# Kernel optimization log

Hardware: AMD Instinct MI355X
Metric: run time of the kernel (lower is better)

## Reference

```python
import jax, jax.numpy as jnp
import numpy as np

NUM_HEADS = 8
OUT_DIM = 32


def setup_inputs() -> dict:
    key = jax.random.key(0)
    k1, k2, k3, k4 = jax.random.split(key, 4)
    B, N, IN = 2048, 64, 256
    h_i_list = jax.random.normal(k1, (B, N, IN), dtype=jnp.float32)
    h_j_list = jax.random.normal(k2, (B, N, IN), dtype=jnp.float32)
    # Linear weight, applied as x @ W (in_dim, num_heads*out_dim)
    W = jax.random.normal(k3, (IN, NUM_HEADS * OUT_DIM), dtype=jnp.float32) * (1.0 / np.sqrt(IN))
    W_att = jax.random.normal(k4, (1, NUM_HEADS, OUT_DIM), dtype=jnp.float32) * 0.1
    return {"h_i_list": h_i_list, "h_j_list": h_j_list, "W": W, "W_att": W_att}


def reference(h_i_list, h_j_list, W, W_att):
    B, N, _ = h_i_list.shape
    H, D = NUM_HEADS, OUT_DIM
    # [B, N, H, D]
    proj_neigh = (h_j_list @ W).reshape(B, N, H, D)
    proj_self = (h_i_list @ W).reshape(B, N, H, D)
    # attention logits: leakyReLU(sum over feature dim) -> [B, N, H]
    e_ij = jax.nn.leaky_relu(((proj_neigh + proj_self) * W_att[None]).sum(-1), 0.2)
    # softmax over neighbor dim (dim=1)
    alpha = jax.nn.softmax(e_ij, axis=1)  # [B, N, H]
    # weighted neighbor sum -> [B, H, D]
    weight_sum = jnp.einsum("bnh,bnhd->bhd", alpha, proj_neigh)
    # concat=True: [B, 1, H*D]
    h_new = weight_sum.reshape(B, 1, H * D)
    return jax.nn.elu(h_new)
```

## Files before the change

kernel.cpp:

```cpp
#include <hip/hip_runtime.h>

#define NN 64
#define IND 256
#define NH 8
#define OD 32

__device__ __forceinline__ unsigned f2bf(float f) {
  unsigned u = __float_as_uint(f);
  return (u + (((u >> 16) & 1u) + 0x7fffu)) >> 16;
}
__device__ __forceinline__ float bflo(unsigned u) { return __uint_as_float(u << 16); }
__device__ __forceinline__ float bfhi(unsigned u) { return __uint_as_float(u & 0xffff0000u); }

__global__ __launch_bounds__(256) void precompute_v(
    const float* __restrict__ W, const float* __restrict__ Watt, float* __restrict__ V) {
  int tid = blockIdx.x * 256 + threadIdx.x;
  if (tid >= IND * NH) return;
  int h = tid >> 8, k = tid & 255;
  float acc = 0.f;
#pragma unroll
  for (int d = 0; d < OD; ++d) acc += W[k * 256 + h * OD + d] * Watt[h * OD + d];
  V[h * 256 + k] = acc;
}

#define V_OFF 33792
#define E_OFF (V_OFF + 8320)
#define SMEM_BYTES (E_OFF + 2048)

__global__ __launch_bounds__(256, 3) void gat_fused(
    const float* __restrict__ Xi, const float* __restrict__ Xj,
    const float* __restrict__ W, const float* __restrict__ V,
    float* __restrict__ out) {
  __shared__ __align__(16) unsigned char smem[SMEM_BYTES];
  unsigned* s_pk = (unsigned*)smem;
  float* v_f = (float*)(smem + V_OFF);
  float* e_f = (float*)(smem + E_OFF);
  float* alpha_f = v_f;
  float* pp_f = v_f;
  float* yp_f = (float*)smem;

  const int t = threadIdx.x;
  const int b = blockIdx.x;
  const int w = t >> 6, l = t & 63;
  const int g = l >> 3, h = l & 7;

  const float4* Xi4 = (const float4*)Xi + (size_t)b * (NN * IND / 4) + w * 1024;
  const float4* Xj4 = (const float4*)Xj + (size_t)b * (NN * IND / 4) + w * 1024;

  {
    const float4* V4 = (const float4*)V;
    float4 vs[8];
#pragma unroll
    for (int r = 0; r < 8; ++r) vs[r] = V4[r * 64 + l];
#pragma unroll
    for (int r = 0; r < 8; ++r) *(float4*)(v_f + r * 260 + 4 * l) = vs[r];
  }

  float4 xj[16], xi[16];
#pragma unroll
  for (int i = 0; i < 16; ++i) {
    xj[i] = Xj4[i * 64 + l];
    xi[i] = Xi4[i * 64 + l];
  }
#pragma unroll
  for (int i = 0; i < 16; ++i) {
    float4 a = xj[i], c = xi[i];
    unsigned p0 = f2bf(a.x + c.x) | (f2bf(a.y + c.y) << 16);
    unsigned p1 = f2bf(a.z + c.z) | (f2bf(a.w + c.w) << 16);
    *(uint2*)(s_pk + (w * 16 + i) * 132 + l * 2) = make_uint2(p0, p1);
  }

  float er[2];
#pragma unroll
  for (int pp = 0; pp < 2; ++pp) {
    int n = w * 16 + g + 8 * pp;
    const uint4* srow = (const uint4*)(s_pk + n * 132);
    const float4* vrow = (const float4*)(v_f + h * 260);
    float acc = 0.f;
#pragma unroll 8
    for (int kk = 0; kk < 32; ++kk) {
      uint4 sp = srow[kk];
      float4 va = vrow[2 * kk], vb = vrow[2 * kk + 1];
      acc += bflo(sp.x) * va.x + bfhi(sp.x) * va.y + bflo(sp.y) * va.z + bfhi(sp.y) * va.w
           + bflo(sp.z) * vb.x + bfhi(sp.z) * vb.y + bflo(sp.w) * vb.z + bfhi(sp.w) * vb.w;
    }
    er[pp] = acc >= 0.f ? acc : 0.2f * acc;
    e_f[n * 8 + h] = er[pp];
  }
  __syncthreads();

  float m = -3.4e38f;
#pragma unroll
  for (int q = 0; q < 8; ++q) m = fmaxf(m, e_f[(g * 8 + q) * 8 + h]);
  m = fmaxf(m, __shfl_xor(m, 8, 64));
  m = fmaxf(m, __shfl_xor(m, 16, 64));
  m = fmaxf(m, __shfl_xor(m, 32, 64));
  float ssum = 0.f;
#pragma unroll
  for (int q = 0; q < 8; ++q) ssum += __expf(e_f[(g * 8 + q) * 8 + h] - m);
  ssum += __shfl_xor(ssum, 8, 64);
  ssum += __shfl_xor(ssum, 16, 64);
  ssum += __shfl_xor(ssum, 32, 64);
  float rinv = 1.f / ssum;

#pragma unroll
  for (int pp = 0; pp < 2; ++pp) {
    int n = w * 16 + g + 8 * pp;
    alpha_f[n * 8 + h] = __expf(er[pp] - m) * rinv;
  }

  float4 acc4[8];
#pragma unroll
  for (int hh = 0; hh < 8; ++hh) acc4[hh] = make_float4(0.f, 0.f, 0.f, 0.f);
#pragma unroll
  for (int i = 0; i < 16; ++i) {
    int n = w * 16 + i;
    float4 a0 = *(const float4*)(alpha_f + n * 8);
    float4 a1 = *(const float4*)(alpha_f + n * 8 + 4);
    float al[8] = {a0.x, a0.y, a0.z, a0.w, a1.x, a1.y, a1.z, a1.w};
    float4 x = xj[i];
#pragma unroll
    for (int hh = 0; hh < 8; ++hh) {
      acc4[hh].x += al[hh] * x.x;
      acc4[hh].y += al[hh] * x.y;
      acc4[hh].z += al[hh] * x.z;
      acc4[hh].w += al[hh] * x.w;
    }
  }
#pragma unroll
  for (int hh = 0; hh < 8; ++hh)
    *(float4*)(yp_f + (w * 8 + hh) * 260 + 4 * l) = acc4[hh];
  __syncthreads();

  {
    const float* ypb = yp_f + g * 260;
    const float4* W4 = (const float4*)W;
    float4 acc = make_float4(0.f, 0.f, 0.f, 0.f);
    int k0 = w * 64;
#pragma unroll 8
    for (int kk = 0; kk < 64; ++kk) {
      int k = k0 + kk;
      float yv = ypb[k] + ypb[2080 + k] + ypb[4160 + k] + ypb[6240 + k];
      float4 wv = W4[k * 64 + l];
      acc.x += yv * wv.x;
      acc.y += yv * wv.y;
      acc.z += yv * wv.z;
      acc.w += yv * wv.w;
    }
    *(float4*)(pp_f + w * 256 + 4 * l) = acc;
  }
  __syncthreads();

  {
    float s = pp_f[t] + pp_f[256 + t] + pp_f[512 + t] + pp_f[768 + t];
    out[(size_t)b * 256 + t] = s > 0.f ? s : (__expf(s) - 1.f);
  }
}

extern "C" void kernel_launch(void* const* d_in, const int* in_sizes, int n_in,
                              void* d_out, int out_size, void* d_ws, size_t ws_size,
                              hipStream_t stream) {
  const float* Xi = (const float*)d_in[0];
  const float* Xj = (const float*)d_in[1];
  const float* W = (const float*)d_in[2];
  const float* Watt = (const float*)d_in[3];
  float* out = (float*)d_out;
  float* V = (float*)d_ws;
  int B = in_sizes[0] / (NN * IND);
  precompute_v<<<(IND * NH + 255) / 256, 256, 0, stream>>>(W, Watt, V);
  gat_fused<<<B, 256, 0, stream>>>(Xi, Xj, W, V, out);
}
```

Before: 304.9 us.

## Pack V to bf16, stage Xi loads in halves, raise occupancy to 4 blocks

V is now stored in shared memory as packed bf16 instead of fp32, which shrinks the V region so the per-block LDS footprint drops enough for four resident blocks per CU. The Xi tile is loaded in two halves of eight float4s to cut register pressure, and launch bounds are raised to 4 blocks per CU. The e_f score array is padded to a stride of 9 to avoid LDS bank conflicts in the softmax reads. The trade-offs are extra bf16 rounding on V in the logit dot product and less memory-level parallelism from the split Xi loads.

```diff
diff --git a/kernel.cpp b/kernel.cpp
--- a/kernel.cpp
+++ b/kernel.cpp
@@ -24,19 +24,19 @@
 }
 
 #define V_OFF 33792
-#define E_OFF (V_OFF + 8320)
-#define SMEM_BYTES (E_OFF + 2048)
+#define E_OFF (V_OFF + 4224)
+#define SMEM_BYTES (E_OFF + 2304)
 
-__global__ __launch_bounds__(256, 3) void gat_fused(
+__global__ __launch_bounds__(256, 4) void gat_fused(
     const float* __restrict__ Xi, const float* __restrict__ Xj,
     const float* __restrict__ W, const float* __restrict__ V,
     float* __restrict__ out) {
   __shared__ __align__(16) unsigned char smem[SMEM_BYTES];
   unsigned* s_pk = (unsigned*)smem;
-  float* v_f = (float*)(smem + V_OFF);
+  unsigned* v_pk = (unsigned*)(smem + V_OFF);
   float* e_f = (float*)(smem + E_OFF);
-  float* alpha_f = v_f;
-  float* pp_f = v_f;
+  float* alpha_f = (float*)(smem + V_OFF);
+  float* pp_f = (float*)(smem + V_OFF);
   float* yp_f = (float*)smem;
 
   const int t = threadIdx.x;
@@ -49,25 +49,31 @@
 
   {
     const float4* V4 = (const float4*)V;
-    float4 vs[8];
 #pragma unroll
-    for (int r = 0; r < 8; ++r) vs[r] = V4[r * 64 + l];
-#pragma unroll
-    for (int r = 0; r < 8; ++r) *(float4*)(v_f + r * 260 + 4 * l) = vs[r];
+    for (int r = 0; r < 8; ++r) {
+      float4 vv = V4[r * 64 + l];
+      unsigned p0 = f2bf(vv.x) | (f2bf(vv.y) << 16);
+      unsigned p1 = f2bf(vv.z) | (f2bf(vv.w) << 16);
+      *(uint2*)(v_pk + r * 132 + 2 * l) = make_uint2(p0, p1);
+    }
   }
 
-  float4 xj[16], xi[16];
+  float4 xj[16];
 #pragma unroll
-  for (int i = 0; i < 16; ++i) {
-    xj[i] = Xj4[i * 64 + l];
-    xi[i] = Xi4[i * 64 + l];
-  }
+  for (int i = 0; i < 16; ++i) xj[i] = Xj4[i * 64 + l];
 #pragma unroll
-  for (int i = 0; i < 16; ++i) {
-    float4 a = xj[i], c = xi[i];
-    unsigned p0 = f2bf(a.x + c.x) | (f2bf(a.y + c.y) << 16);
-    unsigned p1 = f2bf(a.z + c.z) | (f2bf(a.w + c.w) << 16);
-    *(uint2*)(s_pk + (w * 16 + i) * 132 + l * 2) = make_uint2(p0, p1);
+  for (int c = 0; c < 2; ++c) {
+    float4 xi[8];
+#pragma unroll
+    for (int i = 0; i < 8; ++i) xi[i] = Xi4[(c * 8 + i) * 64 + l];
+#pragma unroll
+    for (int i = 0; i < 8; ++i) {
+      int r = c * 8 + i;
+      float4 a = xj[r], ci = xi[i];
+      unsigned p0 = f2bf(a.x + ci.x) | (f2bf(a.y + ci.y) << 16);
+      unsigned p1 = f2bf(a.z + ci.z) | (f2bf(a.w + ci.w) << 16);
+      *(uint2*)(s_pk + (w * 16 + r) * 132 + l * 2) = make_uint2(p0, p1);
+    }
   }
 
   float er[2];
@@ -75,29 +81,31 @@
   for (int pp = 0; pp < 2; ++pp) {
     int n = w * 16 + g + 8 * pp;
     const uint4* srow = (const uint4*)(s_pk + n * 132);
-    const float4* vrow = (const float4*)(v_f + h * 260);
+    const uint4* vrow = (const uint4*)(v_pk + h * 132);
     float acc = 0.f;
 #pragma unroll 8
     for (int kk = 0; kk < 32; ++kk) {
       uint4 sp = srow[kk];
-      float4 va = vrow[2 * kk], vb = vrow[2 * kk + 1];
-      acc += bflo(sp.x) * va.x + bfhi(sp.x) * va.y + bflo(sp.y) * va.z + bfhi(sp.y) * va.w
-           + bflo(sp.z) * vb.x + bfhi(sp.z) * vb.y + bflo(sp.w) * vb.z + bfhi(sp.w) * vb.w;
+      uint4 vp = vrow[kk];
+      acc += bflo(sp.x) * bflo(vp.x) + bfhi(sp.x) * bfhi(vp.x)
+           + bflo(sp.y) * bflo(vp.y) + bfhi(sp.y) * bfhi(vp.y)
+           + bflo(sp.z) * bflo(vp.z) + bfhi(sp.z) * bfhi(vp.z)
+           + bflo(sp.w) * bflo(vp.w) + bfhi(sp.w) * bfhi(vp.w);
     }
     er[pp] = acc >= 0.f ? acc : 0.2f * acc;
-    e_f[n * 8 + h] = er[pp];
+    e_f[n * 9 + h] = er[pp];
   }
   __syncthreads();
 
   float m = -3.4e38f;
 #pragma unroll
-  for (int q = 0; q < 8; ++q) m = fmaxf(m, e_f[(g * 8 + q) * 8 + h]);
+  for (int q = 0; q < 8; ++q) m = fmaxf(m, e_f[(g * 8 + q) * 9 + h]);
   m = fmaxf(m, __shfl_xor(m, 8, 64));
   m = fmaxf(m, __shfl_xor(m, 16, 64));
   m = fmaxf(m, __shfl_xor(m, 32, 64));
   float ssum = 0.f;
 #pragma unroll
-  for (int q = 0; q < 8; ++q) ssum += __expf(e_f[(g * 8 + q) * 8 + h] - m);
+  for (int q = 0; q < 8; ++q) ssum += __expf(e_f[(g * 8 + q) * 9 + h] - m);
   ssum += __shfl_xor(ssum, 8, 64);
   ssum += __shfl_xor(ssum, 16, 64);
   ssum += __shfl_xor(ssum, 32, 64);
```

After: 325.6 us. 6.8% more time.
